# Optimization experiments

Hardware: AMD Instinct MI355X
Metric: run time of the kernel (lower is better)

Reference implementation:

```python
import jax, jax.numpy as jnp
import numpy as np

N = 50000      # num_nodes
E = 400000     # num_edges
H = 64         # h_dim
R = 200        # num_rels
B = 8          # num_bases (block-diagonal decomposition)


def setup_inputs() -> dict:
    ks = jax.random.split(jax.random.key(0), 10)
    s = 1.0 / np.sqrt(H).astype(np.float32)
    return {
        "emb":     jax.random.normal(ks[0], (N, H), jnp.float32),
        "norm":    jax.random.uniform(ks[1], (E, 1), jnp.float32),
        "eps":     jax.random.normal(ks[2], (N, H), jnp.float32),
        "w1":      jax.random.normal(ks[3], (R, B * 8 * 8), jnp.float32) * s,
        "loop_w1": jax.random.normal(ks[4], (H, H), jnp.float32) * s,
        "b1":      jnp.zeros((H,), jnp.float32),
        "w2":      jax.random.normal(ks[5], (R, B * 8 * 16), jnp.float32) * s,
        "loop_w2": jax.random.normal(ks[6], (H, 2 * H), jnp.float32) * s,
        "b2":      jnp.zeros((2 * H,), jnp.float32),
        "h_ids":   jnp.arange(N, dtype=jnp.int32),
        "src":     jax.random.randint(ks[7], (E,), 0, N, jnp.int32),
        "dst":     jax.random.randint(ks[8], (E,), 0, N, jnp.int32),
        "rel":     jax.random.randint(ks[9], (E,), 0, R, jnp.int32),
    }


def bdd_conv(feat, src, dst, rel, norm, weight, loop_w, bias, out_feat):
    # RelGraphConv with 'bdd' regularizer: per-edge relation-indexed
    # block-diagonal weight gather, bmm message, norm scale, scatter-add,
    # then bias + self-loop.
    n_edges = src.shape[0]
    sub_in = feat.shape[1] // B
    sub_out = out_feat // B
    w = weight[rel].reshape(n_edges, B, sub_in, sub_out)   # gather per edge
    x = feat[src].reshape(n_edges, B, sub_in)
    msg = jnp.einsum('ebi,ebio->ebo', x, w).reshape(n_edges, out_feat) * norm
    agg = jax.ops.segment_sum(msg, dst, num_segments=feat.shape[0])
    return agg + bias + feat @ loop_w


def reference(emb, norm, eps, w1, loop_w1, b1, w2, loop_w2, b2,
              h_ids, src, dst, rel):
    feat = emb[h_ids]                                       # embedding lookup
    h1 = jax.nn.relu(bdd_conv(feat, src, dst, rel, norm, w1, loop_w1, b1, H))
    h2 = bdd_conv(h1, src, dst, rel, norm, w2, loop_w2, b2, 2 * H)
    m, raw_v = jnp.split(h2, 2, axis=-1)                    # gaussian_parameters
    v = jax.nn.softplus(raw_v) + 1e-8
    return m + jnp.sqrt(v) * eps                            # reparameterize
```

## Files before the change

kernel.cpp:

```cpp
#include <hip/hip_runtime.h>
#include <math.h>


typedef __attribute__((ext_vector_type(8))) short bf16x8;
typedef __attribute__((ext_vector_type(4))) float f32x4;
typedef __attribute__((ext_vector_type(2))) _Float16 h2;

__device__ __forceinline__ int bcasti(int v, int l) { return __builtin_amdgcn_readlane(v, l); }
__device__ __forceinline__ float bcastf(float v, int l) {
    return __int_as_float(__builtin_amdgcn_readlane(__float_as_int(v), l));
}
__device__ __forceinline__ unsigned short f2bf(float f) {
    unsigned u = __float_as_uint(f);
    return (unsigned short)((u + 0x7FFFu + ((u >> 16) & 1u)) >> 16);
}
__device__ __forceinline__ unsigned short f2h(float f) {
    return __builtin_bit_cast(unsigned short, (_Float16)f);
}
__device__ __forceinline__ float bfs(unsigned short s) { return __uint_as_float((unsigned)s << 16); }
__device__ __forceinline__ h2 uh2(unsigned u) { return __builtin_bit_cast(h2, u); }

__device__ __forceinline__ void gload_lds16(const void* g, void* l) {
    __builtin_amdgcn_global_load_lds(
        (const __attribute__((address_space(1))) unsigned int*)g,
        (__attribute__((address_space(3))) unsigned int*)l, 16, 0, 0);
}

__global__ void hist(const int* __restrict__ dst, int* __restrict__ deg, int e) {
    int i = blockIdx.x * blockDim.x + threadIdx.x;
    if (i < e) atomicAdd(&deg[dst[i]], 1);
}

__global__ void scan_part(const int* __restrict__ deg, int* __restrict__ bsum, int n) {
    __shared__ int sm[256];
    int t = threadIdx.x, g = blockIdx.x * 256 + t;
    sm[t] = (g < n) ? deg[g] : 0;
    __syncthreads();
    for (int d = 128; d > 0; d >>= 1) {
        if (t < d) sm[t] += sm[t + d];
        __syncthreads();
    }
    if (t == 0) bsum[blockIdx.x] = sm[0];
}

__global__ void scan_bsum(int* __restrict__ bsum, int* __restrict__ off, int nb, int n) {
    __shared__ int sm[256];
    int t = threadIdx.x;
    int v = (t < nb) ? bsum[t] : 0;
    sm[t] = v;
    __syncthreads();
    for (int d = 1; d < 256; d <<= 1) {
        int u = (t >= d) ? sm[t - d] : 0;
        __syncthreads();
        sm[t] += u;
        __syncthreads();
    }
    if (t < nb) bsum[t] = sm[t] - v;
    if (t == 255) off[n] = sm[255];
}

__global__ void scan_write(const int* __restrict__ deg, const int* __restrict__ bsum,
                           int* __restrict__ off, int n) {
    __shared__ int sm[256];
    int t = threadIdx.x, g = blockIdx.x * 256 + t;
    int v = (g < n) ? deg[g] : 0;
    sm[t] = v;
    __syncthreads();
    for (int d = 1; d < 256; d <<= 1) {
        int u = (t >= d) ? sm[t - d] : 0;
        __syncthreads();
        sm[t] += u;
        __syncthreads();
    }
    if (g < n) off[g] = bsum[blockIdx.x] + sm[t] - v;
}

__global__ void scatter_pack(const int* __restrict__ src, const int* __restrict__ dst,
                             const int* __restrict__ rel, const float* __restrict__ norm,
                             const int* __restrict__ h_ids, const int* __restrict__ off,
                             int* __restrict__ fil, unsigned* __restrict__ packA,
                             unsigned* __restrict__ packB, float* __restrict__ norm_s, int e) {
    int i = blockIdx.x * blockDim.x + threadIdx.x;
    if (i >= e) return;
    int d = dst[i];
    int p = off[d] + atomicAdd(&fil[d], 1);
    unsigned rhi = (unsigned)rel[i] << 16;
    int s = src[i];
    packA[p] = (unsigned)h_ids[s] | rhi;
    packB[p] = (unsigned)s | rhi;
    norm_s[p] = norm[i];
}

__global__ void cvt_all(const float* __restrict__ w1, const float* __restrict__ w2,
                        const float* __restrict__ emb, unsigned short* __restrict__ w1h,
                        unsigned short* __restrict__ w2h, unsigned short* __restrict__ embh,
                        int n1, int n2, int ne) {
    int i = blockIdx.x * blockDim.x + threadIdx.x;
    if (i < n1) w1h[i] = f2h(w1[i]);
    else if (i < n1 + n2) w2h[i - n1] = f2h(w2[i - n1]);
    else if (i < n1 + n2 + ne) embh[i - n1 - n2] = f2bf(emb[i - n1 - n2]);
}

__global__ __launch_bounds__(256) void
gemm1_mfma(const unsigned short* __restrict__ embh, const int* __restrict__ h_ids,
           const float* __restrict__ lw1, const float* __restrict__ b1,
           unsigned short* __restrict__ h1bh, int n_nodes) {
    int w = threadIdx.x >> 6, l = threadIdx.x & 63;
    int lr = l & 15, lq = l >> 4;
    int rt = blockIdx.x;
    bf16x8 bfr[2];
    int coln = w * 16 + lr;
#pragma unroll
    for (int kb = 0; kb < 2; ++kb)
#pragma unroll
        for (int jj = 0; jj < 8; ++jj)
            bfr[kb][jj] = (short)f2bf(lw1[(kb * 32 + lq * 8 + jj) * 64 + coln]);
    int nrow = rt * 16 + lr;
    if (nrow >= n_nodes) nrow = n_nodes - 1;
    const unsigned short* arow = embh + (long)h_ids[nrow] * 64 + lq * 8;
    bf16x8 af0 = *(const bf16x8*)arow;
    bf16x8 af1 = *(const bf16x8*)(arow + 32);
    f32x4 acc = {0.f, 0.f, 0.f, 0.f};
    acc = __builtin_amdgcn_mfma_f32_16x16x32_bf16(af0, bfr[0], acc, 0, 0, 0);
    acc = __builtin_amdgcn_mfma_f32_16x16x32_bf16(af1, bfr[1], acc, 0, 0, 0);
    float bb = b1[coln];
#pragma unroll
    for (int r = 0; r < 4; ++r) {
        int row = rt * 16 + lq * 4 + r;
        if (row < n_nodes) h1bh[(long)row * 64 + coln] = f2bf(acc[r] + bb);
    }
}

__global__ __launch_bounds__(256) void
gemm2_mfma(const unsigned short* __restrict__ h1h, const float* __restrict__ lw2,
           const float* __restrict__ b2, unsigned short* __restrict__ h2bh, int n_nodes) {
    int w = threadIdx.x >> 6, l = threadIdx.x & 63;
    int lr = l & 15, lq = l >> 4;
    int rt = blockIdx.x;
    bf16x8 bfr[2][2];
    int col0 = (2 * w) * 16 + lr, col1 = (2 * w + 1) * 16 + lr;
#pragma unroll
    for (int kb = 0; kb < 2; ++kb)
#pragma unroll
        for (int jj = 0; jj < 8; ++jj) {
            int k = kb * 32 + lq * 8 + jj;
            bfr[0][kb][jj] = (short)f2bf(lw2[k * 128 + col0]);
            bfr[1][kb][jj] = (short)f2bf(lw2[k * 128 + col1]);
        }
    int nrow = rt * 16 + lr;
    if (nrow >= n_nodes) nrow = n_nodes - 1;
    bf16x8 af0 = *(const bf16x8*)(h1h + (long)nrow * 64 + lq * 8);
    bf16x8 af1 = *(const bf16x8*)(h1h + (long)nrow * 64 + 32 + lq * 8);
    f32x4 acc0 = {0.f, 0.f, 0.f, 0.f}, acc1 = {0.f, 0.f, 0.f, 0.f};
    acc0 = __builtin_amdgcn_mfma_f32_16x16x32_bf16(af0, bfr[0][0], acc0, 0, 0, 0);
    acc0 = __builtin_amdgcn_mfma_f32_16x16x32_bf16(af1, bfr[0][1], acc0, 0, 0, 0);
    acc1 = __builtin_amdgcn_mfma_f32_16x16x32_bf16(af0, bfr[1][0], acc1, 0, 0, 0);
    acc1 = __builtin_amdgcn_mfma_f32_16x16x32_bf16(af1, bfr[1][1], acc1, 0, 0, 0);
    float bb0 = b2[col0], bb1 = b2[col1];
#pragma unroll
    for (int r = 0; r < 4; ++r) {
        int row = rt * 16 + lq * 4 + r;
        if (row < n_nodes) {
            h2bh[(long)row * 128 + col0] = f2bf(acc0[r] + bb0);
            h2bh[(long)row * 128 + col1] = f2bf(acc1[r] + bb1);
        }
    }
}

__device__ __forceinline__ float reduce8(float a0, float a1, float a2, float a3,
                                         float a4, float a5, float a6, float a7, int i) {
    int p1 = i & 1, p2 = (i >> 1) & 1, p3 = (i >> 2) & 1;
    float ka, sb, u0, u1, u2, u3, w0, w1;
    ka = p1 ? a1 : a0; sb = p1 ? a0 : a1; u0 = ka + __shfl_xor(sb, 1, 64);
    ka = p1 ? a3 : a2; sb = p1 ? a2 : a3; u1 = ka + __shfl_xor(sb, 1, 64);
    ka = p1 ? a5 : a4; sb = p1 ? a4 : a5; u2 = ka + __shfl_xor(sb, 1, 64);
    ka = p1 ? a7 : a6; sb = p1 ? a6 : a7; u3 = ka + __shfl_xor(sb, 1, 64);
    ka = p2 ? u1 : u0; sb = p2 ? u0 : u1; w0 = ka + __shfl_xor(sb, 2, 64);
    ka = p2 ? u3 : u2; sb = p2 ? u2 : u3; w1 = ka + __shfl_xor(sb, 2, 64);
    ka = p3 ? w1 : w0; sb = p3 ? w0 : w1;
    return ka + __shfl_xor(sb, 4, 64);
}

__global__ __launch_bounds__(256) void
edge1(const unsigned short* __restrict__ embh, const unsigned short* __restrict__ w1h,
      const unsigned short* __restrict__ h1bh, const int* __restrict__ off,
      const unsigned* __restrict__ packA, const float* __restrict__ norm_s,
      unsigned short* __restrict__ h1h, int n_nodes) {
    __shared__ unsigned short xstage[4][8][64];
    int tid = threadIdx.x;
    int w = tid >> 6, j = tid & 63, i = j & 7;
    int cl = j >> 3, il = j & 7;
    int n = blockIdx.x * 4 + w;
    if (n >= n_nodes) return;
    unsigned short* xsw = &xstage[w][0][0];
    float base = bfs(h1bh[(long)n * 64 + j]);
    h2 acc[4];
#pragma unroll
    for (int q = 0; q < 4; ++q) acc[q] = (h2){(_Float16)0.f, (_Float16)0.f};
    int e0 = off[n], e1v = off[n + 1];
    const long woff = (long)j * 8;
    for (int win = e0; win < e1v; win += 64) {
        int wcnt = e1v - win; if (wcnt > 64) wcnt = 64;
        unsigned u = (j < wcnt) ? packA[win + j] : 0u;
        float nmv = (j < wcnt) ? norm_s[win + j] : 0.f;
        for (int b8 = 0; b8 < wcnt; b8 += 8) {
            int cnt = wcnt - b8; if (cnt > 8) cnt = 8;
            int uc = __builtin_amdgcn_ds_bpermute((b8 + cl) << 2, (int)u);
            if (cl < cnt)
                gload_lds16(embh + (long)((unsigned)uc & 0xFFFFu) * 64 + (il << 3), xsw);
            asm volatile("s_waitcnt vmcnt(0)" ::: "memory");
            __builtin_amdgcn_sched_barrier(0);
#pragma unroll
            for (int c = 0; c < 8; ++c)
                if (c < cnt) {
                    float nm = bcastf(nmv, b8 + c);
                    int rr = bcasti((int)u, b8 + c) >> 16;
                    uint4 wd = *(const uint4*)(w1h + (long)rr * 512 + woff);
                    _Float16 xh = (_Float16)(bfs(xsw[(c << 6) + j]) * nm);
                    h2 xh2 = {xh, xh};
                    acc[0] += xh2 * uh2(wd.x);
                    acc[1] += xh2 * uh2(wd.y);
                    acc[2] += xh2 * uh2(wd.z);
                    acc[3] += xh2 * uh2(wd.w);
                }
        }
    }
    float agg = reduce8((float)acc[0].x, (float)acc[0].y, (float)acc[1].x, (float)acc[1].y,
                        (float)acc[2].x, (float)acc[2].y, (float)acc[3].x, (float)acc[3].y, i);
    h1h[(long)n * 64 + j] = f2bf(fmaxf(base + agg, 0.f));
}

__global__ __launch_bounds__(256) void
edge2(const unsigned short* __restrict__ h1h, const unsigned short* __restrict__ w2h,
      const unsigned short* __restrict__ h2bh, const float* __restrict__ eps,
      const int* __restrict__ off, const unsigned* __restrict__ packB,
      const float* __restrict__ norm_s, float* __restrict__ out, int n_nodes) {
    __shared__ unsigned short xstage[4][8][64];
    int tid = threadIdx.x;
    int w = tid >> 6, j = tid & 63;
    int i = j & 7, b = j >> 3;
    int o1 = b * 16 + i, o2 = o1 + 8;
    int cl = j >> 3, il = j & 7;
    int n = blockIdx.x * 4 + w;
    if (n >= n_nodes) return;
    unsigned short* xsw = &xstage[w][0][0];
    float base1 = bfs(h2bh[(long)n * 128 + o1]);
    float base2 = bfs(h2bh[(long)n * 128 + o2]);
    h2 acc[8];
#pragma unroll
    for (int q = 0; q < 8; ++q) acc[q] = (h2){(_Float16)0.f, (_Float16)0.f};
    int e0 = off[n], e1v = off[n + 1];
    const long woff = (long)j * 16;
    for (int win = e0; win < e1v; win += 64) {
        int wcnt = e1v - win; if (wcnt > 64) wcnt = 64;
        unsigned u = (j < wcnt) ? packB[win + j] : 0u;
        float nmv = (j < wcnt) ? norm_s[win + j] : 0.f;
        for (int b8 = 0; b8 < wcnt; b8 += 8) {
            int cnt = wcnt - b8; if (cnt > 8) cnt = 8;
            int uc = __builtin_amdgcn_ds_bpermute((b8 + cl) << 2, (int)u);
            if (cl < cnt)
                gload_lds16(h1h + (long)((unsigned)uc & 0xFFFFu) * 64 + (il << 3), xsw);
            asm volatile("s_waitcnt vmcnt(0)" ::: "memory");
            __builtin_amdgcn_sched_barrier(0);
#pragma unroll
            for (int c = 0; c < 8; ++c)
                if (c < cnt) {
                    float nm = bcastf(nmv, b8 + c);
                    int rr = bcasti((int)u, b8 + c) >> 16;
                    const uint4* p = (const uint4*)(w2h + (long)rr * 1024 + woff);
                    uint4 wa = p[0], wb = p[1];
                    _Float16 xh = (_Float16)(bfs(xsw[(c << 6) + j]) * nm);
                    h2 xh2 = {xh, xh};
                    acc[0] += xh2 * uh2(wa.x);
                    acc[1] += xh2 * uh2(wa.y);
                    acc[2] += xh2 * uh2(wa.z);
                    acc[3] += xh2 * uh2(wa.w);
                    acc[4] += xh2 * uh2(wb.x);
                    acc[5] += xh2 * uh2(wb.y);
                    acc[6] += xh2 * uh2(wb.z);
                    acc[7] += xh2 * uh2(wb.w);
                }
        }
    }
    float r1 = reduce8((float)acc[0].x, (float)acc[0].y, (float)acc[1].x, (float)acc[1].y,
                       (float)acc[2].x, (float)acc[2].y, (float)acc[3].x, (float)acc[3].y, i);
    float r2 = reduce8((float)acc[4].x, (float)acc[4].y, (float)acc[5].x, (float)acc[5].y,
                       (float)acc[6].x, (float)acc[6].y, (float)acc[7].x, (float)acc[7].y, i);
    float v1 = r1 + base1;
    float v2 = r2 + base2;
    float p1 = __shfl_xor(v1, 32, 64);
    float p2 = __shfl_xor(v2, 32, 64);
    if (j < 32) {
        long basep = (long)n * 64;
        float sp1 = (p1 > 20.f) ? p1 : log1pf(expf(p1));
        float sp2 = (p2 > 20.f) ? p2 : log1pf(expf(p2));
        out[basep + o1] = fmaf(sqrtf(sp1 + 1e-8f), eps[basep + o1], v1);
        out[basep + o2] = fmaf(sqrtf(sp2 + 1e-8f), eps[basep + o2], v2);
    }
}

extern "C" void kernel_launch(void* const* d_in, const int* in_sizes, int n_in,
                              void* d_out, int out_size, void* d_ws, size_t ws_size,
                              hipStream_t stream) {
    const float* emb   = (const float*)d_in[0];
    const float* norm  = (const float*)d_in[1];
    const float* eps   = (const float*)d_in[2];
    const float* w1    = (const float*)d_in[3];
    const float* lw1   = (const float*)d_in[4];
    const float* b1    = (const float*)d_in[5];
    const float* w2    = (const float*)d_in[6];
    const float* lw2   = (const float*)d_in[7];
    const float* b2    = (const float*)d_in[8];
    const int*   h_ids = (const int*)d_in[9];
    const int*   src   = (const int*)d_in[10];
    const int*   dst   = (const int*)d_in[11];
    const int*   rel   = (const int*)d_in[12];
    float* out = (float*)d_out;

    int n_nodes = in_sizes[0] / 64;
    int n_edges = in_sizes[10];
    int nw1 = in_sizes[3];
    int nw2 = in_sizes[6];
    int ne  = in_sizes[0];

    char* ws = (char*)d_ws;
    unsigned short* h1bh = (unsigned short*)ws;       ws += (size_t)n_nodes * 64 * 2;
    unsigned short* h1h  = (unsigned short*)ws;       ws += (size_t)n_nodes * 64 * 2;
    unsigned short* h2bh = (unsigned short*)ws;       ws += (size_t)n_nodes * 128 * 2;
    unsigned short* embh = (unsigned short*)ws;       ws += (size_t)ne * 2;
    unsigned short* w1h  = (unsigned short*)ws;       ws += (size_t)nw1 * 2;
    unsigned short* w2h  = (unsigned short*)ws;       ws += (size_t)nw2 * 2;
    unsigned* pkA = (unsigned*)ws;                    ws += (size_t)n_edges * 4;
    unsigned* pkB = (unsigned*)ws;                    ws += (size_t)n_edges * 4;
    float* norm_s = (float*)ws;                       ws += (size_t)n_edges * 4;
    int*   deg    = (int*)ws;                         ws += (size_t)n_nodes * 4;
    int*   fil    = (int*)ws;                         ws += (size_t)n_nodes * 4;
    int*   off    = (int*)ws;                         ws += (size_t)(n_nodes + 1) * 4;
    int*   bsum   = (int*)ws;

    int blk = 256;
    int nb = (n_nodes + 255) / 256;
    int nt = (n_nodes + 15) / 16;
    int ng = (n_nodes + 3) / 4;
    hipMemsetAsync(deg, 0, (size_t)n_nodes * 8, stream);
    cvt_all<<<(nw1 + nw2 + ne + blk - 1) / blk, blk, 0, stream>>>(w1, w2, emb, w1h, w2h, embh, nw1, nw2, ne);
    hist<<<(n_edges + blk - 1) / blk, blk, 0, stream>>>(dst, deg, n_edges);
    scan_part<<<nb, 256, 0, stream>>>(deg, bsum, n_nodes);
    scan_bsum<<<1, 256, 0, stream>>>(bsum, off, nb, n_nodes);
    scan_write<<<nb, 256, 0, stream>>>(deg, bsum, off, n_nodes);
    scatter_pack<<<(n_edges + blk - 1) / blk, blk, 0, stream>>>(src, dst, rel, norm, h_ids, off, fil, pkA, pkB, norm_s, n_edges);
    gemm1_mfma<<<nt, blk, 0, stream>>>(embh, h_ids, lw1, b1, h1bh, n_nodes);
    edge1<<<ng, blk, 0, stream>>>(embh, w1h, h1bh, off, pkA, norm_s, h1h, n_nodes);
    gemm2_mfma<<<nt, blk, 0, stream>>>(h1h, lw2, b2, h2bh, n_nodes);
    edge2<<<ng, blk, 0, stream>>>(h1h, w2h, h2bh, eps, off, pkB, norm_s, out, n_nodes);
}
```

Baseline: 264.1 us.

## Process two destination nodes per wavefront in edge kernels; fuse histogram into convert

Each wavefront in edge1 and edge2 now handles two consecutive destination nodes, walking their combined CSR edge range and routing each edge into one of two accumulator sets by comparing against the boundary offset. This fills the 8-edge batches and 64-edge windows better, since the average degree is about 8, and halves the number of waves. The degree histogram is folded into the cvt_all kernel, which removes one launch. The cost is twice the accumulator registers, a per-edge branch, and lower parallelism.

```diff
diff --git a/kernel.cpp b/kernel.cpp
--- a/kernel.cpp
+++ b/kernel.cpp
@@ -24,11 +24,6 @@
     __builtin_amdgcn_global_load_lds(
         (const __attribute__((address_space(1))) unsigned int*)g,
         (__attribute__((address_space(3))) unsigned int*)l, 16, 0, 0);
-}
-
-__global__ void hist(const int* __restrict__ dst, int* __restrict__ deg, int e) {
-    int i = blockIdx.x * blockDim.x + threadIdx.x;
-    if (i < e) atomicAdd(&deg[dst[i]], 1);
 }
 
 __global__ void scan_part(const int* __restrict__ deg, int* __restrict__ bsum, int n) {
@@ -94,11 +89,13 @@
 __global__ void cvt_all(const float* __restrict__ w1, const float* __restrict__ w2,
                         const float* __restrict__ emb, unsigned short* __restrict__ w1h,
                         unsigned short* __restrict__ w2h, unsigned short* __restrict__ embh,
-                        int n1, int n2, int ne) {
+                        const int* __restrict__ dst, int* __restrict__ deg,
+                        int n1, int n2, int ne, int e) {
     int i = blockIdx.x * blockDim.x + threadIdx.x;
     if (i < n1) w1h[i] = f2h(w1[i]);
     else if (i < n1 + n2) w2h[i - n1] = f2h(w2[i - n1]);
     else if (i < n1 + n2 + ne) embh[i - n1 - n2] = f2bf(emb[i - n1 - n2]);
+    if (i < e) atomicAdd(&deg[dst[i]], 1);
 }
 
 __global__ __launch_bounds__(256) void
@@ -190,17 +187,21 @@
     int tid = threadIdx.x;
     int w = tid >> 6, j = tid & 63, i = j & 7;
     int cl = j >> 3, il = j & 7;
-    int n = blockIdx.x * 4 + w;
-    if (n >= n_nodes) return;
+    int n0 = (blockIdx.x * 4 + w) * 2;
+    if (n0 >= n_nodes) return;
+    bool has1 = (n0 + 1) < n_nodes;
     unsigned short* xsw = &xstage[w][0][0];
-    float base = bfs(h1bh[(long)n * 64 + j]);
-    h2 acc[4];
-#pragma unroll
-    for (int q = 0; q < 4; ++q) acc[q] = (h2){(_Float16)0.f, (_Float16)0.f};
-    int e0 = off[n], e1v = off[n + 1];
+    float base0 = bfs(h1bh[(long)n0 * 64 + j]);
+    float base1 = has1 ? bfs(h1bh[(long)(n0 + 1) * 64 + j]) : 0.f;
+    h2 ac0[4], ac1[4];
+#pragma unroll
+    for (int q = 0; q < 4; ++q) { ac0[q] = (h2){(_Float16)0.f, (_Float16)0.f}; ac1[q] = ac0[q]; }
+    int e00 = off[n0];
+    int mid = has1 ? off[n0 + 1] : off[n0 + 1];
+    int e11 = has1 ? off[n0 + 2] : mid;
     const long woff = (long)j * 8;
-    for (int win = e0; win < e1v; win += 64) {
-        int wcnt = e1v - win; if (wcnt > 64) wcnt = 64;
+    for (int win = e00; win < e11; win += 64) {
+        int wcnt = e11 - win; if (wcnt > 64) wcnt = 64;
         unsigned u = (j < wcnt) ? packA[win + j] : 0u;
         float nmv = (j < wcnt) ? norm_s[win + j] : 0.f;
         for (int b8 = 0; b8 < wcnt; b8 += 8) {
@@ -218,16 +219,28 @@
                     uint4 wd = *(const uint4*)(w1h + (long)rr * 512 + woff);
                     _Float16 xh = (_Float16)(bfs(xsw[(c << 6) + j]) * nm);
                     h2 xh2 = {xh, xh};
-                    acc[0] += xh2 * uh2(wd.x);
-                    acc[1] += xh2 * uh2(wd.y);
-                    acc[2] += xh2 * uh2(wd.z);
-                    acc[3] += xh2 * uh2(wd.w);
+                    if (win + b8 + c < mid) {
+                        ac0[0] += xh2 * uh2(wd.x);
+                        ac0[1] += xh2 * uh2(wd.y);
+                        ac0[2] += xh2 * uh2(wd.z);
+                        ac0[3] += xh2 * uh2(wd.w);
+                    } else {
+                        ac1[0] += xh2 * uh2(wd.x);
+                        ac1[1] += xh2 * uh2(wd.y);
+                        ac1[2] += xh2 * uh2(wd.z);
+                        ac1[3] += xh2 * uh2(wd.w);
+                    }
                 }
         }
     }
-    float agg = reduce8((float)acc[0].x, (float)acc[0].y, (float)acc[1].x, (float)acc[1].y,
-                        (float)acc[2].x, (float)acc[2].y, (float)acc[3].x, (float)acc[3].y, i);
-    h1h[(long)n * 64 + j] = f2bf(fmaxf(base + agg, 0.f));
+    float agg0 = reduce8((float)ac0[0].x, (float)ac0[0].y, (float)ac0[1].x, (float)ac0[1].y,
+                         (float)ac0[2].x, (float)ac0[2].y, (float)ac0[3].x, (float)ac0[3].y, i);
+    h1h[(long)n0 * 64 + j] = f2bf(fmaxf(base0 + agg0, 0.f));
+    if (has1) {
+        float agg1 = reduce8((float)ac1[0].x, (float)ac1[0].y, (float)ac1[1].x, (float)ac1[1].y,
+                             (float)ac1[2].x, (float)ac1[2].y, (float)ac1[3].x, (float)ac1[3].y, i);
+        h1h[(long)(n0 + 1) * 64 + j] = f2bf(fmaxf(base1 + agg1, 0.f));
+    }
 }
 
 __global__ __launch_bounds__(256) void
@@ -241,18 +254,23 @@
     int i = j & 7, b = j >> 3;
     int o1 = b * 16 + i, o2 = o1 + 8;
     int cl = j >> 3, il = j & 7;
-    int n = blockIdx.x * 4 + w;
-    if (n >= n_nodes) return;
+    int n0 = (blockIdx.x * 4 + w) * 2;
+    if (n0 >= n_nodes) return;
+    bool has1 = (n0 + 1) < n_nodes;
     unsigned short* xsw = &xstage[w][0][0];
-    float base1 = bfs(h2bh[(long)n * 128 + o1]);
-    float base2 = bfs(h2bh[(long)n * 128 + o2]);
-    h2 acc[8];
-#pragma unroll
-    for (int q = 0; q < 8; ++q) acc[q] = (h2){(_Float16)0.f, (_Float16)0.f};
-    int e0 = off[n], e1v = off[n + 1];
+    float b0a = bfs(h2bh[(long)n0 * 128 + o1]);
+    float b0b = bfs(h2bh[(long)n0 * 128 + o2]);
+    float b1a = has1 ? bfs(h2bh[(long)(n0 + 1) * 128 + o1]) : 0.f;
+    float b1b = has1 ? bfs(h2bh[(long)(n0 + 1) * 128 + o2]) : 0.f;
+    h2 ac0[8], ac1[8];
+#pragma unroll
+    for (int q = 0; q < 8; ++q) { ac0[q] = (h2){(_Float16)0.f, (_Float16)0.f}; ac1[q] = ac0[q]; }
+    int e00 = off[n0];
+    int mid = off[n0 + 1];
+    int e11 = has1 ? off[n0 + 2] : mid;
     const long woff = (long)j * 16;
-    for (int win = e0; win < e1v; win += 64) {
-        int wcnt = e1v - win; if (wcnt > 64) wcnt = 64;
+    for (int win = e00; win < e11; win += 64) {
+        int wcnt = e11 - win; if (wcnt > 64) wcnt = 64;
         unsigned u = (j < wcnt) ? packB[win + j] : 0u;
         float nmv = (j < wcnt) ? norm_s[win + j] : 0.f;
         for (int b8 = 0; b8 < wcnt; b8 += 8) {
@@ -271,31 +289,50 @@
                     uint4 wa = p[0], wb = p[1];
                     _Float16 xh = (_Float16)(bfs(xsw[(c << 6) + j]) * nm);
                     h2 xh2 = {xh, xh};
-                    acc[0] += xh2 * uh2(wa.x);
-                    acc[1] += xh2 * uh2(wa.y);
-                    acc[2] += xh2 * uh2(wa.z);
-                    acc[3] += xh2 * uh2(wa.w);
-                    acc[4] += xh2 * uh2(wb.x);
-                    acc[5] += xh2 * uh2(wb.y);
-                    acc[6] += xh2 * uh2(wb.z);
-                    acc[7] += xh2 * uh2(wb.w);
+                    if (win + b8 + c < mid) {
+                        ac0[0] += xh2 * uh2(wa.x);
+                        ac0[1] += xh2 * uh2(wa.y);
+                        ac0[2] += xh2 * uh2(wa.z);
+                        ac0[3] += xh2 * uh2(wa.w);
+                        ac0[4] += xh2 * uh2(wb.x);
+                        ac0[5] += xh2 * uh2(wb.y);
+                        ac0[6] += xh2 * uh2(wb.z);
+                        ac0[7] += xh2 * uh2(wb.w);
+                    } else {
+                        ac1[0] += xh2 * uh2(wa.x);
+                        ac1[1] += xh2 * uh2(wa.y);
+                        ac1[2] += xh2 * uh2(wa.z);
+                        ac1[3] += xh2 * uh2(wa.w);
+                        ac1[4] += xh2 * uh2(wb.x);
+                        ac1[5] += xh2 * uh2(wb.y);
+                        ac1[6] += xh2 * uh2(wb.z);
+                        ac1[7] += xh2 * uh2(wb.w);
+                    }
                 }
         }
     }
-    float r1 = reduce8((float)acc[0].x, (float)acc[0].y, (float)acc[1].x, (float)acc[1].y,
-                       (float)acc[2].x, (float)acc[2].y, (float)acc[3].x, (float)acc[3].y, i);
-    float r2 = reduce8((float)acc[4].x, (float)acc[4].y, (float)acc[5].x, (float)acc[5].y,
-                       (float)acc[6].x, (float)acc[6].y, (float)acc[7].x, (float)acc[7].y, i);
-    float v1 = r1 + base1;
-    float v2 = r2 + base2;
-    float p1 = __shfl_xor(v1, 32, 64);
-    float p2 = __shfl_xor(v2, 32, 64);
-    if (j < 32) {
-        long basep = (long)n * 64;
-        float sp1 = (p1 > 20.f) ? p1 : log1pf(expf(p1));
-        float sp2 = (p2 > 20.f) ? p2 : log1pf(expf(p2));
-        out[basep + o1] = fmaf(sqrtf(sp1 + 1e-8f), eps[basep + o1], v1);
-        out[basep + o2] = fmaf(sqrtf(sp2 + 1e-8f), eps[basep + o2], v2);
+#pragma unroll
+    for (int nn = 0; nn < 2; ++nn) {
+        if (nn == 1 && !has1) break;
+        h2* ac = (nn == 0) ? ac0 : ac1;
+        float bma = (nn == 0) ? b0a : b1a;
+        float bmb = (nn == 0) ? b0b : b1b;
+        long node = n0 + nn;
+        float r1 = reduce8((float)ac[0].x, (float)ac[0].y, (float)ac[1].x, (float)ac[1].y,
+                           (float)ac[2].x, (float)ac[2].y, (float)ac[3].x, (float)ac[3].y, i);
+        float r2 = reduce8((float)ac[4].x, (float)ac[4].y, (float)ac[5].x, (float)ac[5].y,
+                           (float)ac[6].x, (float)ac[6].y, (float)ac[7].x, (float)ac[7].y, i);
+        float v1 = r1 + bma;
+        float v2 = r2 + bmb;
+        float p1 = __shfl_xor(v1, 32, 64);
+        float p2 = __shfl_xor(v2, 32, 64);
+        if (j < 32) {
+            long basep = node * 64;
+            float sp1 = (p1 > 20.f) ? p1 : log1pf(expf(p1));
+            float sp2 = (p2 > 20.f) ? p2 : log1pf(expf(p2));
+            out[basep + o1] = fmaf(sqrtf(sp1 + 1e-8f), eps[basep + o1], v1);
+            out[basep + o2] = fmaf(sqrtf(sp2 + 1e-8f), eps[basep + o2], v2);
+        }
     }
 }
 
@@ -341,16 +378,18 @@
     int blk = 256;
     int nb = (n_nodes + 255) / 256;
     int nt = (n_nodes + 15) / 16;
-    int ng = (n_nodes + 3) / 4;
+    int ng2 = (n_nodes + 7) / 8;
+    int ncv = nw1 + nw2 + ne;
+    if (ncv < n_edges) ncv = n_edges;
     hipMemsetAsync(deg, 0, (size_t)n_nodes * 8, stream);
-    cvt_all<<<(nw1 + nw2 + ne + blk - 1) / blk, blk, 0, stream>>>(w1, w2, emb, w1h, w2h, embh, nw1, nw2, ne);
-    hist<<<(n_edges + blk - 1) / blk, blk, 0, stream>>>(dst, deg, n_edges);
+    cvt_all<<<(ncv + blk - 1) / blk, blk, 0, stream>>>(w1, w2, emb, w1h, w2h, embh,
+                                                       dst, deg, nw1, nw2, ne, n_edges);
     scan_part<<<nb, 256, 0, stream>>>(deg, bsum, n_nodes);
     scan_bsum<<<1, 256, 0, stream>>>(bsum, off, nb, n_nodes);
     scan_write<<<nb, 256, 0, stream>>>(deg, bsum, off, n_nodes);
     scatter_pack<<<(n_edges + blk - 1) / blk, blk, 0, stream>>>(src, dst, rel, norm, h_ids, off, fil, pkA, pkB, norm_s, n_edges);
     gemm1_mfma<<<nt, blk, 0, stream>>>(embh, h_ids, lw1, b1, h1bh, n_nodes);
-    edge1<<<ng, blk, 0, stream>>>(embh, w1h, h1bh, off, pkA, norm_s, h1h, n_nodes);
+    edge1<<<ng2, blk, 0, stream>>>(embh, w1h, h1bh, off, pkA, norm_s, h1h, n_nodes);
     gemm2_mfma<<<nt, blk, 0, stream>>>(h1h, lw2, b2, h2bh, n_nodes);
-    edge2<<<ng, blk, 0, stream>>>(h1h, w2h, h2bh, eps, off, pkB, norm_s, out, n_nodes);
-}
+    edge2<<<ng2, blk, 0, stream>>>(h1h, w2h, h2bh, eps, off, pkB, norm_s, out, n_nodes);
+}
```

Result: slower. 282.3 us (+6.9%).
